# Kernel optimization log

Hardware: AMD Instinct MI355X
Metric: run time of the kernel (lower is better)

Reference implementation:

```python
import jax, jax.numpy as jnp
import numpy as np

N_NODES = 50000
N_EDGES = 600000
F_IN = 128
DIM_H = 256
N_CLASSES = 40
BN_EPS = 1e-5


def setup_inputs() -> dict:
    key = jax.random.key(0)
    ks = jax.random.split(key, 10)
    x = jax.random.normal(ks[0], (N_NODES, F_IN), dtype=jnp.float32)
    edge_index = jax.random.randint(ks[1], (2, N_EDGES), 0, N_NODES, dtype=jnp.int64)
    s1 = 1.0 / np.sqrt(F_IN)
    s2 = 1.0 / np.sqrt(DIM_H)
    W1 = jax.random.uniform(ks[2], (F_IN, DIM_H), jnp.float32, -s1, s1)
    b1 = jax.random.uniform(ks[3], (DIM_H,), jnp.float32, -s1, s1)
    gamma = jnp.ones((DIM_H,), jnp.float32)
    beta = jnp.zeros((DIM_H,), jnp.float32)
    W2 = jax.random.uniform(ks[4], (DIM_H, DIM_H), jnp.float32, -s2, s2)
    b2 = jax.random.uniform(ks[5], (DIM_H,), jnp.float32, -s2, s2)
    Wlin = jax.random.uniform(ks[6], (DIM_H, N_CLASSES), jnp.float32, -s2, s2)
    blin = jax.random.uniform(ks[7], (N_CLASSES,), jnp.float32, -s2, s2)
    return {"x": x, "edge_index": edge_index, "W1": W1, "b1": b1,
            "gamma": gamma, "beta": beta, "W2": W2, "b2": b2,
            "Wlin": Wlin, "blin": blin}


def reference(x, edge_index, W1, b1, gamma, beta, W2, b2, Wlin, blin):
    src, dst = edge_index[0], edge_index[1]
    # GIN sum aggregation: agg[i] = sum_{(j->i)} x[j]; eps = 0 (default)
    agg = jax.ops.segment_sum(x[src], dst, num_segments=N_NODES)  # [N, F_IN]
    h = x + agg
    # MLP: Linear -> BatchNorm1d (training-mode batch stats) -> ReLU -> Linear -> ReLU
    h = h @ W1 + b1                               # [N, DIM_H]
    mean = jnp.mean(h, axis=0)
    var = jnp.var(h, axis=0)                      # biased, as torch BN uses for normalization
    h = (h - mean) * jax.lax.rsqrt(var + BN_EPS) * gamma + beta
    h = jax.nn.relu(h)
    h = jax.nn.relu(h @ W2 + b2)                  # MLP final ReLU; outer x.relu() is idempotent
    return h @ Wlin + blin                        # [N, N_CLASSES]
```

## Files before the change

### kernel.cpp

```cpp
#include <hip/hip_runtime.h>

#define F_IN 128
#define DIM_H 256
#define N_CLASSES 40
#define BN_EPS 1e-5f
#define M_PAD 50176

typedef short bf16x8 __attribute__((ext_vector_type(8)));
typedef float f32x4 __attribute__((ext_vector_type(4)));

__device__ __forceinline__ unsigned short f2bf(float f) {
    union { float f; unsigned u; } v; v.f = f;
    unsigned r = v.u + 0x7fff + ((v.u >> 16) & 1);
    return (unsigned short)(r >> 16);
}
__device__ __forceinline__ float bf2f(unsigned short u) {
    union { unsigned u; float f; } v; v.u = ((unsigned)u) << 16;
    return v.f;
}
__device__ __forceinline__ float4 bf2f4(ushort4 u) {
    return make_float4(bf2f(u.x), bf2f(u.y), bf2f(u.z), bf2f(u.w));
}

__global__ void hist_kernel(const int* __restrict__ dst, int* __restrict__ hist, int nE) {
    int e = blockIdx.x * blockDim.x + threadIdx.x;
    if (e >= nE) return;
    atomicAdd(&hist[dst[e]], 1);
}

__global__ void scan_blocks_kernel(const int* __restrict__ hist,
                                   int* __restrict__ blockSums, int M) {
    __shared__ int lds[256];
    int t = threadIdx.x;
    int i = blockIdx.x * 256 + t;
    lds[t] = (i < M) ? hist[i] : 0;
    __syncthreads();
    for (int off = 128; off > 0; off >>= 1) {
        if (t < off) lds[t] += lds[t + off];
        __syncthreads();
    }
    if (t == 0) blockSums[blockIdx.x] = lds[0];
}

__global__ void scan_offsets_kernel(const int* __restrict__ blockSums,
                                    int* __restrict__ blockOffs,
                                    int nB, int* __restrict__ start, int M, int nE) {
    __shared__ int lds[256];
    int t = threadIdx.x;
    int orig = (t < nB) ? blockSums[t] : 0;
    lds[t] = orig;
    __syncthreads();
    for (int off = 1; off < 256; off <<= 1) {
        int v = (t >= off) ? lds[t - off] : 0;
        __syncthreads();
        lds[t] += v;
        __syncthreads();
    }
    if (t < nB) blockOffs[t] = lds[t] - orig;
    if (t == 0) start[M] = nE;
}

__global__ void scan_final_kernel(const int* __restrict__ hist,
                                  const int* __restrict__ blockOffs,
                                  int* __restrict__ start, int M) {
    __shared__ int lds[256];
    int t = threadIdx.x;
    int i = blockIdx.x * 256 + t;
    int orig = (i < M) ? hist[i] : 0;
    lds[t] = orig;
    __syncthreads();
    for (int off = 1; off < 256; off <<= 1) {
        int v = (t >= off) ? lds[t - off] : 0;
        __syncthreads();
        lds[t] += v;
        __syncthreads();
    }
    if (i < M) start[i] = blockOffs[blockIdx.x] + lds[t] - orig;
}

__global__ void fill_kernel(const int* __restrict__ src, const int* __restrict__ dst,
                            const int* __restrict__ start, int* __restrict__ cursor,
                            int* __restrict__ order, int nE) {
    int e = blockIdx.x * blockDim.x + threadIdx.x;
    if (e >= nE) return;
    int d = dst[e];
    int pos = start[d] + atomicAdd(&cursor[d], 1);
    order[pos] = src[e];
}

__global__ void prep_kernel(const float* __restrict__ x, unsigned short* __restrict__ xb,
                            const float* __restrict__ W1, const float* __restrict__ W2,
                            const float* __restrict__ Wl,
                            unsigned short* __restrict__ W1t,
                            unsigned short* __restrict__ W2t,
                            unsigned short* __restrict__ Wlt, int XQ) {
    int idx = blockIdx.x * 256 + threadIdx.x;
    if (idx < XQ) {
        float4 v = ((const float4*)x)[idx];
        ushort4 o;
        o.x = f2bf(v.x); o.y = f2bf(v.y); o.z = f2bf(v.z); o.w = f2bf(v.w);
        ((ushort4*)xb)[idx] = o;
        return;
    }
    int j = idx - XQ;
    if (j < 32768) {
        int n = j >> 7, k = j & 127;
        W1t[j] = f2bf(W1[k * DIM_H + n]);
    } else if (j < 32768 + 65536) {
        int i = j - 32768;
        int n = i >> 8, k = i & 255;
        W2t[i] = f2bf(W2[k * DIM_H + n]);
    } else if (j < 32768 + 65536 + 16384) {
        int i = j - 98304;
        int n = i >> 8, k = i & 255;
        Wlt[i] = f2bf((n < N_CLASSES) ? Wl[k * N_CLASSES + n] : 0.f);
    }
}

__global__ void gather_agg_kernel(const float* __restrict__ x,
                                  const unsigned short* __restrict__ xb,
                                  const int* __restrict__ order,
                                  const int* __restrict__ start,
                                  unsigned short* __restrict__ A1, int M) {
    int node = blockIdx.x * 8 + (threadIdx.x >> 5);
    if (node >= M) return;
    int lane = threadIdx.x & 31;
    const ushort4* xv = (const ushort4*)xb;
    float4 a0 = ((const float4*)x)[(size_t)node * 32 + lane];
    float4 a1 = make_float4(0.f, 0.f, 0.f, 0.f);
    float4 a2 = a1, a3 = a1;
    int e0 = start[node], e1 = start[node + 1];
    int e = e0;
    for (; e + 4 <= e1; e += 4) {
        int s0 = order[e], s1 = order[e + 1], s2 = order[e + 2], s3 = order[e + 3];
        float4 v0 = bf2f4(xv[(size_t)s0 * 32 + lane]);
        float4 v1 = bf2f4(xv[(size_t)s1 * 32 + lane]);
        float4 v2 = bf2f4(xv[(size_t)s2 * 32 + lane]);
        float4 v3 = bf2f4(xv[(size_t)s3 * 32 + lane]);
        a0.x += v0.x; a0.y += v0.y; a0.z += v0.z; a0.w += v0.w;
        a1.x += v1.x; a1.y += v1.y; a1.z += v1.z; a1.w += v1.w;
        a2.x += v2.x; a2.y += v2.y; a2.z += v2.z; a2.w += v2.w;
        a3.x += v3.x; a3.y += v3.y; a3.z += v3.z; a3.w += v3.w;
    }
    for (; e < e1; ++e) {
        float4 v = bf2f4(xv[(size_t)order[e] * 32 + lane]);
        a1.x += v.x; a1.y += v.y; a1.z += v.z; a1.w += v.w;
    }
    float4 t;
    t.x = (a0.x + a1.x) + (a2.x + a3.x);
    t.y = (a0.y + a1.y) + (a2.y + a3.y);
    t.z = (a0.z + a1.z) + (a2.z + a3.z);
    t.w = (a0.w + a1.w) + (a2.w + a3.w);
    ushort4 o;
    o.x = f2bf(t.x); o.y = f2bf(t.y); o.z = f2bf(t.z); o.w = f2bf(t.w);
    ((ushort4*)A1)[(size_t)node * 32 + lane] = o;
}

__global__ void bn_reduce_kernel(const float* __restrict__ partials, int R,
                                 const float* __restrict__ gamma,
                                 const float* __restrict__ beta,
                                 float* __restrict__ scale,
                                 float* __restrict__ shift, int M) {
    __shared__ float ls[256], lss[256];
    int c = blockIdx.x, t = threadIdx.x;
    float s = 0.f, ss = 0.f;
    for (int r = t; r < R; r += 256) {
        s += partials[(long)r * 512 + c];
        ss += partials[(long)r * 512 + 256 + c];
    }
    ls[t] = s; lss[t] = ss;
    __syncthreads();
    for (int o = 128; o > 0; o >>= 1) {
        if (t < o) { ls[t] += ls[t + o]; lss[t] += lss[t + o]; }
        __syncthreads();
    }
    if (t == 0) {
        float inv = 1.0f / (float)M;
        float mean = ls[0] * inv;
        float var = lss[0] * inv - mean * mean;
        float sc = gamma[c] * rsqrtf(var + BN_EPS);
        scale[c] = sc;
        shift[c] = beta[c] - mean * sc;
    }
}

template <int WM, int WN, int K, int MODE>
__global__ __launch_bounds__(256) void mfma_gemm(
    const unsigned short* __restrict__ A,
    const unsigned short* __restrict__ Bt,
    const float* __restrict__ bias,
    void* __restrict__ Cout,
    const float* __restrict__ scale,
    const float* __restrict__ shift,
    float* __restrict__ partials,
    int M, int Nout) {
    constexpr int BM = WM * 64, BN = WN * 64;
    constexpr int S = K / 32;
    constexpr int PITCH = 40;
    constexpr int ACH = BM / 64;
    constexpr int BCH = BN / 64;

    __shared__ __align__(16) unsigned short As[2][BM * PITCH];
    __shared__ __align__(16) unsigned short Bs[2][BN * PITCH];

    int tid = threadIdx.x;
    int wave = tid >> 6, lane = tid & 63;
    int wm = wave / WN, wn = wave % WN;
    int l15 = lane & 15, q = lane >> 4;
    long row0 = (long)blockIdx.y * BM;
    long col0 = (long)blockIdx.x * BN;

    bf16x8 ar[ACH], br[BCH];

    auto loadAB = [&](int s) {
#pragma unroll
        for (int i = 0; i < ACH; ++i) {
            int ch = tid + i * 256;
            int m = ch >> 2, c = ch & 3;
            ar[i] = *(const bf16x8*)(A + (row0 + m) * K + s * 32 + c * 8);
        }
#pragma unroll
        for (int i = 0; i < BCH; ++i) {
            int ch = tid + i * 256;
            int m = ch >> 2, c = ch & 3;
            br[i] = *(const bf16x8*)(Bt + (col0 + m) * K + s * 32 + c * 8);
        }
    };

    auto writeAB = [&](int buf, int s) {
#pragma unroll
        for (int i = 0; i < ACH; ++i) {
            int ch = tid + i * 256;
            int m = ch >> 2, c = ch & 3;
            bf16x8 v = ar[i];
            if (MODE == 1) {
                int kb = s * 32 + c * 8;
                float4 sc0 = *(const float4*)(scale + kb);
                float4 sc1 = *(const float4*)(scale + kb + 4);
                float4 sh0 = *(const float4*)(shift + kb);
                float4 sh1 = *(const float4*)(shift + kb + 4);
                float scv[8] = {sc0.x, sc0.y, sc0.z, sc0.w, sc1.x, sc1.y, sc1.z, sc1.w};
                float shv[8] = {sh0.x, sh0.y, sh0.z, sh0.w, sh1.x, sh1.y, sh1.z, sh1.w};
#pragma unroll
                for (int j = 0; j < 8; ++j) {
                    float f = bf2f((unsigned short)v[j]);
                    f = fmaxf(f * scv[j] + shv[j], 0.f);
                    v[j] = (short)f2bf(f);
                }
            }
            *(bf16x8*)(&As[buf][m * PITCH + c * 8]) = v;
        }
#pragma unroll
        for (int i = 0; i < BCH; ++i) {
            int ch = tid + i * 256;
            int m = ch >> 2, c = ch & 3;
            *(bf16x8*)(&Bs[buf][m * PITCH + c * 8]) = br[i];
        }
    };

    f32x4 acc[4][4] = {};

    loadAB(0);
    writeAB(0, 0);
#pragma unroll
    for (int s = 0; s < S; ++s) {
        if (s + 1 < S) loadAB(s + 1);
        __syncthreads();
        int buf = s & 1;
        bf16x8 af[4], bfr[4];
#pragma unroll
        for (int mt = 0; mt < 4; ++mt)
            af[mt] = *(const bf16x8*)(&As[buf][(wm * 64 + mt * 16 + l15) * PITCH + q * 8]);
#pragma unroll
        for (int nt = 0; nt < 4; ++nt)
            bfr[nt] = *(const bf16x8*)(&Bs[buf][(wn * 64 + nt * 16 + l15) * PITCH + q * 8]);
#pragma unroll
        for (int mt = 0; mt < 4; ++mt)
#pragma unroll
            for (int nt = 0; nt < 4; ++nt)
                acc[mt][nt] = __builtin_amdgcn_mfma_f32_16x16x32_bf16(
                    af[mt], bfr[nt], acc[mt][nt], 0, 0, 0);
        if (s + 1 < S) writeAB((s + 1) & 1, s + 1);
    }

#pragma unroll
    for (int nt = 0; nt < 4; ++nt) {
        long col = col0 + wn * 64 + nt * 16 + l15;
        float b = (MODE == 2) ? ((col < Nout) ? bias[col] : 0.f) : bias[col];
        float s = 0.f, ss = 0.f;
#pragma unroll
        for (int mt = 0; mt < 4; ++mt) {
#pragma unroll
            for (int r = 0; r < 4; ++r) {
                long row = row0 + wm * 64 + mt * 16 + q * 4 + r;
                float v = acc[mt][nt][r] + b;
                if (row < M) {
                    if (MODE == 0) {
                        ((unsigned short*)Cout)[row * DIM_H + col] = f2bf(v);
                        s += v; ss += v * v;
                    } else if (MODE == 1) {
                        ((unsigned short*)Cout)[row * DIM_H + col] = f2bf(fmaxf(v, 0.f));
                    } else {
                        if (col < Nout) ((float*)Cout)[row * Nout + col] = v;
                    }
                }
            }
        }
        if (MODE == 0) {
            s += __shfl_xor(s, 16, 64);  s += __shfl_xor(s, 32, 64);
            ss += __shfl_xor(ss, 16, 64); ss += __shfl_xor(ss, 32, 64);
            if (lane < 16) {
                long pr = (long)blockIdx.y * WM + wm;
                partials[pr * 512 + col] = s;
                partials[pr * 512 + 256 + col] = ss;
            }
        }
    }
}

extern "C" void kernel_launch(void* const* d_in, const int* in_sizes, int n_in,
                              void* d_out, int out_size, void* d_ws, size_t ws_size,
                              hipStream_t stream) {
    const float* x     = (const float*)d_in[0];
    const int*   ei    = (const int*)d_in[1];
    const float* W1    = (const float*)d_in[2];
    const float* b1    = (const float*)d_in[3];
    const float* gamma = (const float*)d_in[4];
    const float* beta  = (const float*)d_in[5];
    const float* W2    = (const float*)d_in[6];
    const float* b2    = (const float*)d_in[7];
    const float* Wlin  = (const float*)d_in[8];
    const float* blin  = (const float*)d_in[9];
    float* out = (float*)d_out;

    int M  = in_sizes[0] / F_IN;
    int nE = in_sizes[1] / 2;
    const int* srcIdx = ei;
    const int* dstIdx = ei + nE;
    int nB = (M + 255) / 256;
    int g12y = (M + 127) / 128;
    int g3y  = (M + 255) / 256;
    int Rpart = g12y * 2;
    int XQ = M * 32;

    unsigned short* A1bf  = (unsigned short*)d_ws;
    unsigned short* h1bf  = A1bf + (size_t)M_PAD * F_IN;
    unsigned short* h2bf  = h1bf + (size_t)M_PAD * DIM_H;
    unsigned short* xb    = h2bf + (size_t)M_PAD * DIM_H;
    unsigned short* W1t   = xb + (size_t)M_PAD * F_IN;
    unsigned short* W2t   = W1t + DIM_H * F_IN;
    unsigned short* Wlt   = W2t + DIM_H * DIM_H;
    float*          partials = (float*)(Wlt + 64 * DIM_H);
    float*          scale = partials + (size_t)800 * 512;
    float*          shift = scale + DIM_H;
    int*            hist  = (int*)(shift + DIM_H);
    int*            cursor= hist + M;
    int*            start = cursor + M;
    int*            blockSums = start + (M + 1);
    int*            blockOffs = blockSums + 256;
    int*            order = blockOffs + 256;

    hipMemsetAsync(hist, 0, (size_t)2 * M * sizeof(int), stream);

    int tB = 256;
    hist_kernel<<<(nE + tB - 1) / tB, tB, 0, stream>>>(dstIdx, hist, nE);
    scan_blocks_kernel<<<nB, 256, 0, stream>>>(hist, blockSums, M);
    scan_offsets_kernel<<<1, 256, 0, stream>>>(blockSums, blockOffs, nB, start, M, nE);
    scan_final_kernel<<<nB, 256, 0, stream>>>(hist, blockOffs, start, M);
    fill_kernel<<<(nE + tB - 1) / tB, tB, 0, stream>>>(srcIdx, dstIdx, start, cursor, order, nE);
    prep_kernel<<<(XQ + 114688 + 255) / 256, 256, 0, stream>>>(
        x, xb, W1, W2, Wlin, W1t, W2t, Wlt, XQ);
    gather_agg_kernel<<<(M + 7) / 8, 256, 0, stream>>>(x, xb, order, start, A1bf, M);

    mfma_gemm<2, 2, F_IN, 0><<<dim3(2, g12y), 256, 0, stream>>>(
        A1bf, W1t, b1, h1bf, nullptr, nullptr, partials, M, DIM_H);
    bn_reduce_kernel<<<DIM_H, 256, 0, stream>>>(partials, Rpart, gamma, beta, scale, shift, M);
    mfma_gemm<2, 2, DIM_H, 1><<<dim3(2, g12y), 256, 0, stream>>>(
        h1bf, W2t, b2, h2bf, scale, shift, nullptr, M, DIM_H);
    mfma_gemm<4, 1, DIM_H, 2><<<dim3(1, g3y), 256, 0, stream>>>(
        h2bf, Wlt, blin, out, nullptr, nullptr, nullptr, M, N_CLASSES);
}
```

Baseline: 271.7 us.

## Fuse final classifier GEMM into second MLP GEMM via LDS-staged h2 tile

Changes GEMM tiling to 64x256 blocks (one wave per 64 rows covering all 256 columns) so each block holds a full h2 row tile. The second GEMM now writes ReLU(h2) as bf16 into LDS and immediately multiplies by the padded Wlin with MFMA, writing the 40-class output directly. This removes the h2 global write/read round-trip and the third kernel launch. Padding rows of A1/h1 are zeroed in prep. In exchange the fused kernel issues more per-block work and reads Wlin straight from global memory, and the narrower grid gives fewer blocks.

```diff
diff --git a/kernel.cpp b/kernel.cpp
--- a/kernel.cpp
+++ b/kernel.cpp
@@ -93,7 +93,10 @@
                             const float* __restrict__ Wl,
                             unsigned short* __restrict__ W1t,
                             unsigned short* __restrict__ W2t,
-                            unsigned short* __restrict__ Wlt, int XQ) {
+                            unsigned short* __restrict__ Wlt,
+                            unsigned short* __restrict__ A1pad,
+                            unsigned short* __restrict__ h1pad,
+                            int XQ) {
     int idx = blockIdx.x * 256 + threadIdx.x;
     if (idx < XQ) {
         float4 v = ((const float4*)x)[idx];
@@ -114,6 +117,10 @@
         int i = j - 98304;
         int n = i >> 8, k = i & 255;
         Wlt[i] = f2bf((n < N_CLASSES) ? Wl[k * N_CLASSES + n] : 0.f);
+    } else if (j < 114688 + 4608) {
+        int i = j - 114688;
+        if (i < 1536) ((ushort4*)A1pad)[i] = make_ushort4(0, 0, 0, 0);
+        else ((ushort4*)h1pad)[i - 1536] = make_ushort4(0, 0, 0, 0);
     }
 }
 
@@ -185,7 +192,7 @@
 }
 
 template <int WM, int WN, int K, int MODE>
-__global__ __launch_bounds__(256) void mfma_gemm(
+__global__ __launch_bounds__(WM* WN * 64) void mfma_gemm(
     const unsigned short* __restrict__ A,
     const unsigned short* __restrict__ Bt,
     const float* __restrict__ bias,
@@ -193,15 +200,23 @@
     const float* __restrict__ scale,
     const float* __restrict__ shift,
     float* __restrict__ partials,
-    int M, int Nout) {
+    const unsigned short* __restrict__ Wlt2,
+    const float* __restrict__ bias2,
+    int M) {
+    constexpr int NT = WM * WN * 64;
     constexpr int BM = WM * 64, BN = WN * 64;
     constexpr int S = K / 32;
     constexpr int PITCH = 40;
-    constexpr int ACH = BM / 64;
-    constexpr int BCH = BN / 64;
-
-    __shared__ __align__(16) unsigned short As[2][BM * PITCH];
-    __shared__ __align__(16) unsigned short Bs[2][BN * PITCH];
+    constexpr int ACH = BM * 4 / NT;
+    constexpr int BCH = BN * 4 / NT;
+    constexpr int STAGE = 2 * (BM + BN) * PITCH;
+    constexpr int H2PITCH = 264;
+    constexpr int H2T = (MODE == 1) ? BM * H2PITCH : 0;
+    constexpr int LDSN = STAGE > H2T ? STAGE : H2T;
+
+    __shared__ __align__(16) unsigned short lds[LDSN];
+    unsigned short* AsBase = lds;
+    unsigned short* BsBase = lds + 2 * BM * PITCH;
 
     int tid = threadIdx.x;
     int wave = tid >> 6, lane = tid & 63;
@@ -215,13 +230,13 @@
     auto loadAB = [&](int s) {
 #pragma unroll
         for (int i = 0; i < ACH; ++i) {
-            int ch = tid + i * 256;
+            int ch = tid + i * NT;
             int m = ch >> 2, c = ch & 3;
             ar[i] = *(const bf16x8*)(A + (row0 + m) * K + s * 32 + c * 8);
         }
 #pragma unroll
         for (int i = 0; i < BCH; ++i) {
-            int ch = tid + i * 256;
+            int ch = tid + i * NT;
             int m = ch >> 2, c = ch & 3;
             br[i] = *(const bf16x8*)(Bt + (col0 + m) * K + s * 32 + c * 8);
         }
@@ -230,7 +245,7 @@
     auto writeAB = [&](int buf, int s) {
 #pragma unroll
         for (int i = 0; i < ACH; ++i) {
-            int ch = tid + i * 256;
+            int ch = tid + i * NT;
             int m = ch >> 2, c = ch & 3;
             bf16x8 v = ar[i];
             if (MODE == 1) {
@@ -248,13 +263,13 @@
                     v[j] = (short)f2bf(f);
                 }
             }
-            *(bf16x8*)(&As[buf][m * PITCH + c * 8]) = v;
+            *(bf16x8*)(&AsBase[buf * BM * PITCH + m * PITCH + c * 8]) = v;
         }
 #pragma unroll
         for (int i = 0; i < BCH; ++i) {
-            int ch = tid + i * 256;
+            int ch = tid + i * NT;
             int m = ch >> 2, c = ch & 3;
-            *(bf16x8*)(&Bs[buf][m * PITCH + c * 8]) = br[i];
+            *(bf16x8*)(&BsBase[buf * BN * PITCH + m * PITCH + c * 8]) = br[i];
         }
     };
 
@@ -270,10 +285,10 @@
         bf16x8 af[4], bfr[4];
 #pragma unroll
         for (int mt = 0; mt < 4; ++mt)
-            af[mt] = *(const bf16x8*)(&As[buf][(wm * 64 + mt * 16 + l15) * PITCH + q * 8]);
+            af[mt] = *(const bf16x8*)(&AsBase[buf * BM * PITCH + (wm * 64 + mt * 16 + l15) * PITCH + q * 8]);
 #pragma unroll
         for (int nt = 0; nt < 4; ++nt)
-            bfr[nt] = *(const bf16x8*)(&Bs[buf][(wn * 64 + nt * 16 + l15) * PITCH + q * 8]);
+            bfr[nt] = *(const bf16x8*)(&BsBase[buf * BN * PITCH + (wn * 64 + nt * 16 + l15) * PITCH + q * 8]);
 #pragma unroll
         for (int mt = 0; mt < 4; ++mt)
 #pragma unroll
@@ -283,36 +298,68 @@
         if (s + 1 < S) writeAB((s + 1) & 1, s + 1);
     }
 
-#pragma unroll
-    for (int nt = 0; nt < 4; ++nt) {
-        long col = col0 + wn * 64 + nt * 16 + l15;
-        float b = (MODE == 2) ? ((col < Nout) ? bias[col] : 0.f) : bias[col];
-        float s = 0.f, ss = 0.f;
-#pragma unroll
-        for (int mt = 0; mt < 4; ++mt) {
-#pragma unroll
-            for (int r = 0; r < 4; ++r) {
-                long row = row0 + wm * 64 + mt * 16 + q * 4 + r;
-                float v = acc[mt][nt][r] + b;
-                if (row < M) {
-                    if (MODE == 0) {
+    if (MODE == 0) {
+#pragma unroll
+        for (int nt = 0; nt < 4; ++nt) {
+            long col = col0 + wn * 64 + nt * 16 + l15;
+            float b = bias[col];
+            float s = 0.f, ss = 0.f;
+#pragma unroll
+            for (int mt = 0; mt < 4; ++mt) {
+#pragma unroll
+                for (int r = 0; r < 4; ++r) {
+                    long row = row0 + wm * 64 + mt * 16 + q * 4 + r;
+                    float v = acc[mt][nt][r] + b;
+                    if (row < M) {
                         ((unsigned short*)Cout)[row * DIM_H + col] = f2bf(v);
                         s += v; ss += v * v;
-                    } else if (MODE == 1) {
-                        ((unsigned short*)Cout)[row * DIM_H + col] = f2bf(fmaxf(v, 0.f));
-                    } else {
-                        if (col < Nout) ((float*)Cout)[row * Nout + col] = v;
                     }
                 }
             }
-        }
-        if (MODE == 0) {
             s += __shfl_xor(s, 16, 64);  s += __shfl_xor(s, 32, 64);
             ss += __shfl_xor(ss, 16, 64); ss += __shfl_xor(ss, 32, 64);
             if (lane < 16) {
                 long pr = (long)blockIdx.y * WM + wm;
                 partials[pr * 512 + col] = s;
                 partials[pr * 512 + 256 + col] = ss;
+            }
+        }
+    } else {
+        __syncthreads();
+        unsigned short* h2t = lds;
+#pragma unroll
+        for (int nt = 0; nt < 4; ++nt) {
+            int colL = wn * 64 + nt * 16 + l15;
+            float b = bias[colL];
+#pragma unroll
+            for (int mt = 0; mt < 4; ++mt)
+#pragma unroll
+                for (int r = 0; r < 4; ++r) {
+                    int rowL = mt * 16 + q * 4 + r;
+                    h2t[rowL * H2PITCH + colL] = f2bf(fmaxf(acc[mt][nt][r] + b, 0.f));
+                }
+        }
+        __syncthreads();
+        f32x4 acc3[3] = {};
+#pragma unroll
+        for (int s = 0; s < 8; ++s) {
+            bf16x8 a3 = *(const bf16x8*)(&h2t[(wave * 16 + l15) * H2PITCH + s * 32 + q * 8]);
+#pragma unroll
+            for (int nt = 0; nt < 3; ++nt) {
+                bf16x8 b3 = *(const bf16x8*)(Wlt2 + (nt * 16 + l15) * 256 + s * 32 + q * 8);
+                acc3[nt] = __builtin_amdgcn_mfma_f32_16x16x32_bf16(a3, b3, acc3[nt], 0, 0, 0);
+            }
+        }
+#pragma unroll
+        for (int nt = 0; nt < 3; ++nt) {
+            int col = nt * 16 + l15;
+            if (col < N_CLASSES) {
+                float b = bias2[col];
+#pragma unroll
+                for (int r = 0; r < 4; ++r) {
+                    long row = row0 + wave * 16 + q * 4 + r;
+                    if (row < M) ((float*)Cout)[row * N_CLASSES + col] = acc3[nt][r] + b;
+                }
             }
         }
     }
@@ -338,15 +385,13 @@
     const int* srcIdx = ei;
     const int* dstIdx = ei + nE;
     int nB = (M + 255) / 256;
-    int g12y = (M + 127) / 128;
-    int g3y  = (M + 255) / 256;
-    int Rpart = g12y * 2;
+    int gy = (M + 63) / 64;
+    int Rpart = gy;
     int XQ = M * 32;
 
     unsigned short* A1bf  = (unsigned short*)d_ws;
     unsigned short* h1bf  = A1bf + (size_t)M_PAD * F_IN;
-    unsigned short* h2bf  = h1bf + (size_t)M_PAD * DIM_H;
-    unsigned short* xb    = h2bf + (size_t)M_PAD * DIM_H;
+    unsigned short* xb    = h1bf + (size_t)M_PAD * DIM_H;
     unsigned short* W1t   = xb + (size_t)M_PAD * F_IN;
     unsigned short* W2t   = W1t + DIM_H * F_IN;
     unsigned short* Wlt   = W2t + DIM_H * DIM_H;
@@ -368,15 +413,14 @@
     scan_offsets_kernel<<<1, 256, 0, stream>>>(blockSums, blockOffs, nB, start, M, nE);
     scan_final_kernel<<<nB, 256, 0, stream>>>(hist, blockOffs, start, M);
     fill_kernel<<<(nE + tB - 1) / tB, tB, 0, stream>>>(srcIdx, dstIdx, start, cursor, order, nE);
-    prep_kernel<<<(XQ + 114688 + 255) / 256, 256, 0, stream>>>(
-        x, xb, W1, W2, Wlin, W1t, W2t, Wlt, XQ);
+    prep_kernel<<<(XQ + 114688 + 4608 + 255) / 256, 256, 0, stream>>>(
+        x, xb, W1, W2, Wlin, W1t, W2t, Wlt,
+        A1bf + (size_t)M * F_IN, h1bf + (size_t)M * DIM_H, XQ);
     gather_agg_kernel<<<(M + 7) / 8, 256, 0, stream>>>(x, xb, order, start, A1bf, M);
 
-    mfma_gemm<2, 2, F_IN, 0><<<dim3(2, g12y), 256, 0, stream>>>(
-        A1bf, W1t, b1, h1bf, nullptr, nullptr, partials, M, DIM_H);
+    mfma_gemm<1, 4, F_IN, 0><<<dim3(1, gy), 256, 0, stream>>>(
+        A1bf, W1t, b1, h1bf, nullptr, nullptr, partials, nullptr, nullptr, M);
     bn_reduce_kernel<<<DIM_H, 256, 0, stream>>>(partials, Rpart, gamma, beta, scale, shift, M);
-    mfma_gemm<2, 2, DIM_H, 1><<<dim3(2, g12y), 256, 0, stream>>>(
-        h1bf, W2t, b2, h2bf, scale, shift, nullptr, M, DIM_H);
-    mfma_gemm<4, 1, DIM_H, 2><<<dim3(1, g3y), 256, 0, stream>>>(
-        h2bf, Wlt, blin, out, nullptr, nullptr, nullptr, M, N_CLASSES);
-}
+    mfma_gemm<1, 4, DIM_H, 1><<<dim3(1, gy), 256, 0, stream>>>(
+        h1bf, W2t, b2, out, scale, shift, nullptr, Wlt, blin, M);
+}
```

Result: faster. 252.0 us (-7.3%).
